# Kernel tuning notes

Measured on AMD Instinct MI355X. Metric: run time of the kernel, lower is better.

Reference implementation:

```python
import jax, jax.numpy as jnp
import numpy as np


def setup_inputs() -> dict:
    key = jax.random.key(0)
    k1, k2, k3 = jax.random.split(key, 3)
    b, n, h, d = 2, 2048, 16, 64
    q = jax.random.normal(k1, (b, n, h, d), dtype=jnp.float32)
    k = jax.random.normal(k2, (b, n, h, d), dtype=jnp.float32)
    v = jax.random.normal(k3, (b, n, h, d), dtype=jnp.float32)
    return {"q": q, "k": k, "v": v, "is_causal": 1}


def reference(q, k, v, is_causal):
    # q, k, v: [b, n, h, d]
    b, n, h, d = q.shape
    scale = 1.0 / jnp.sqrt(jnp.asarray(d, dtype=q.dtype))
    # scores: [b, h, n_q, n_k]
    scores = jnp.einsum("bqhd,bkhd->bhqk", q, k) * scale
    if is_causal:
        causal_mask = jnp.triu(jnp.ones((n, n), dtype=bool), k=1)  # True above diagonal
        scores = jnp.where(causal_mask[None, None, :, :], jnp.asarray(-jnp.inf, scores.dtype), scores)
    attn = jax.nn.softmax(scores, axis=-1)
    # output back to [b, n, h, d]
    out = jnp.einsum("bhqk,bkhd->bqhd", attn, v)
    return out
```

## Files before the change

### kernel.cpp

```cpp
#include <hip/hip_runtime.h>
#include <hip/hip_bf16.h>
#include <math.h>

typedef __bf16 bf16x8 __attribute__((ext_vector_type(8)));
typedef __bf16 bf16x4 __attribute__((ext_vector_type(4)));
typedef float  f32x4  __attribute__((ext_vector_type(4)));

#define KVBLK 64
#define HD    64
#define LDK   72
#define LDV   68
#define LDP   72
#define NQT   32

__global__ __launch_bounds__(256, 2)
void fattn_fwd(const float* __restrict__ Q, const float* __restrict__ K,
               const float* __restrict__ V, const int* __restrict__ causal_p,
               float* __restrict__ O, int B, int N, int H) {
  __shared__ alignas(16) __bf16 Kl[KVBLK][LDK];
  __shared__ alignas(16) __bf16 Vl[HD][LDV];
  __shared__ alignas(16) __bf16 Pl[64][LDP];

  const int tid  = threadIdx.x;
  const int wave = tid >> 6;
  const int lane = tid & 63;
  const int lo   = lane & 15;
  const int hi   = lane >> 4;

  const int xA = blockIdx.x;
  const int xB = NQT - 1 - xA;
  const int bh = blockIdx.y;
  const int bb = bh / H;
  const int hh = bh - bb * H;

  const int causal = causal_p[0];
  const int sN = H * HD;

  const float* Qb = Q + (long)bb * N * sN + hh * HD;
  const float* Kb = K + (long)bb * N * sN + hh * HD;
  const float* Vb = V + (long)bb * N * sN + hh * HD;
  float*       Ob = O + (long)bb * N * sN + hh * HD;

  const int tmaxA = causal ? xA : (NQT - 1);
  const int tmaxB = causal ? xB : (NQT - 1);

  const float qscale = 0.125f * 1.44269504088896340736f;
  bf16x8 aq[2][2];
#pragma unroll
  for (int qi = 0; qi < 2; ++qi) {
    const int q0q = ((qi == 0) ? xA : xB) * 64;
    const float* qp = Qb + (long)(q0q + wave * 16 + lo) * sN;
#pragma unroll
    for (int c = 0; c < 2; ++c) {
      f32x4 x0 = *(const f32x4*)(qp + c * 32 + hi * 8);
      f32x4 x1 = *(const f32x4*)(qp + c * 32 + hi * 8 + 4);
      bf16x8 a;
#pragma unroll
      for (int j = 0; j < 4; ++j) {
        a[j]     = (__bf16)(x0[j] * qscale);
        a[j + 4] = (__bf16)(x1[j] * qscale);
      }
      aq[qi][c] = a;
    }
  }

  f32x4 acc[2][4];
  float m_run[2][4], l_run[2][4];
#pragma unroll
  for (int qi = 0; qi < 2; ++qi)
#pragma unroll
    for (int i = 0; i < 4; ++i) {
      acc[qi][i] = (f32x4){0.f, 0.f, 0.f, 0.f};
      m_run[qi][i] = -INFINITY;
      l_run[qi][i] = 0.f;
    }

  f32x4 kreg[4], vreg[4];
  auto issue = [&](int tt) {
    const int k0 = tt * KVBLK;
#pragma unroll
    for (int i = 0; i < 4; ++i) {
      const int flat = tid + i * 256;
      const int r = flat >> 4, c4 = (flat & 15) * 4;
      kreg[i] = *(const f32x4*)(Kb + (long)(k0 + r) * sN + c4);
    }
    const float* vrow = Vb + (long)(k0 + wave * 16 + hi * 4) * sN + lo * 4;
#pragma unroll
    for (int q = 0; q < 4; ++q) vreg[q] = *(const f32x4*)(vrow + (long)q * sN);
  };
  auto wr = [&]() {
#pragma unroll
    for (int i = 0; i < 4; ++i) {
      const int flat = tid + i * 256;
      const int r = flat >> 4, c4 = (flat & 15) * 4;
      bf16x4 kb;
#pragma unroll
      for (int j = 0; j < 4; ++j) kb[j] = (__bf16)kreg[i][j];
      *(bf16x4*)&Kl[r][c4] = kb;
    }
#pragma unroll
    for (int j = 0; j < 4; ++j) {
      bf16x4 vv;
#pragma unroll
      for (int q = 0; q < 4; ++q) vv[q] = (__bf16)vreg[q][j];
      *(bf16x4*)&Vl[lo * 4 + j][wave * 16 + hi * 4] = vv;
    }
  };

  issue(0);
  wr();
  __syncthreads();

  for (int t = 0; t <= tmaxB; ++t) {
    const bool pf = (t < tmaxB);
    if (pf) issue(t + 1);
    const int k0 = t * KVBLK;

#pragma unroll
    for (int qi = 0; qi < 2; ++qi) {
      if (qi == 0 && t > tmaxA) continue;
      const int qt  = (qi == 0) ? xA : xB;
      const int q0q = qt * 64;

      f32x4 s[4];
#pragma unroll
      for (int nt = 0; nt < 4; ++nt) s[nt] = (f32x4){0.f, 0.f, 0.f, 0.f};
#pragma unroll
      for (int c = 0; c < 2; ++c) {
#pragma unroll
        for (int nt = 0; nt < 4; ++nt) {
          bf16x8 b = *(const bf16x8*)&Kl[nt * 16 + lo][c * 32 + hi * 8];
          s[nt] = __builtin_amdgcn_mfma_f32_16x16x32_bf16(aq[qi][c], b, s[nt], 0, 0, 0);
        }
      }

      if (causal && t == qt) {
#pragma unroll
        for (int nt = 0; nt < 4; ++nt) {
          const int kvg = k0 + nt * 16 + lo;
#pragma unroll
          for (int r = 0; r < 4; ++r) {
            const int qg = q0q + wave * 16 + hi * 4 + r;
            if (kvg > qg) s[nt][r] = -INFINITY;
          }
        }
      }

#pragma unroll
      for (int r = 0; r < 4; ++r) {
        float mx = fmaxf(fmaxf(s[0][r], s[1][r]), fmaxf(s[2][r], s[3][r]));
        mx = fmaxf(mx, __shfl_xor(mx, 1));
        mx = fmaxf(mx, __shfl_xor(mx, 2));
        mx = fmaxf(mx, __shfl_xor(mx, 4));
        mx = fmaxf(mx, __shfl_xor(mx, 8));
        const float mnew = fmaxf(m_run[qi][r], mx);
        const float fac  = exp2f(m_run[qi][r] - mnew);
        float ps = 0.f;
#pragma unroll
        for (int nt = 0; nt < 4; ++nt) {
          const float p = exp2f(s[nt][r] - mnew);
          s[nt][r] = p;
          ps += p;
        }
        ps += __shfl_xor(ps, 1);
        ps += __shfl_xor(ps, 2);
        ps += __shfl_xor(ps, 4);
        ps += __shfl_xor(ps, 8);
        l_run[qi][r] = l_run[qi][r] * fac + ps;
        m_run[qi][r] = mnew;
#pragma unroll
        for (int nt = 0; nt < 4; ++nt) acc[qi][nt][r] *= fac;
      }

      asm volatile("s_waitcnt lgkmcnt(0)" ::: "memory");
#pragma unroll
      for (int nt = 0; nt < 4; ++nt)
#pragma unroll
        for (int r = 0; r < 4; ++r)
          Pl[wave * 16 + hi * 4 + r][nt * 16 + lo] = (__bf16)s[nt][r];
      asm volatile("s_waitcnt lgkmcnt(0)" ::: "memory");

#pragma unroll
      for (int c = 0; c < 2; ++c) {
        bf16x8 pa = *(const bf16x8*)&Pl[wave * 16 + lo][c * 32 + hi * 8];
#pragma unroll
        for (int nt = 0; nt < 4; ++nt) {
          const __bf16* vp = &Vl[nt * 16 + lo][c * 32 + hi * 8];
          bf16x4 v0 = *(const bf16x4*)vp;
          bf16x4 v1 = *(const bf16x4*)(vp + 4);
          bf16x8 vb;
#pragma unroll
          for (int j = 0; j < 4; ++j) { vb[j] = v0[j]; vb[j + 4] = v1[j]; }
          acc[qi][nt] = __builtin_amdgcn_mfma_f32_16x16x32_bf16(pa, vb, acc[qi][nt], 0, 0, 0);
        }
      }
    }

    __syncthreads();
    if (pf) wr();
    __syncthreads();
  }

#pragma unroll
  for (int qi = 0; qi < 2; ++qi) {
    const int q0q = ((qi == 0) ? xA : xB) * 64;
    const int qrow = q0q + wave * 16 + hi * 4;
#pragma unroll
    for (int nt = 0; nt < 4; ++nt) {
#pragma unroll
      for (int r = 0; r < 4; ++r) {
        Ob[(long)(qrow + r) * sN + nt * 16 + lo] = acc[qi][nt][r] / l_run[qi][r];
      }
    }
  }
}

extern "C" void kernel_launch(void* const* d_in, const int* in_sizes, int n_in,
                              void* d_out, int out_size, void* d_ws, size_t ws_size,
                              hipStream_t stream) {
  const float* q = (const float*)d_in[0];
  const float* k = (const float*)d_in[1];
  const float* v = (const float*)d_in[2];
  const int* causal = (const int*)d_in[3];
  float* out = (float*)d_out;
  const int B = 2, N = 2048, H = 16;
  dim3 grid(NQT / 2, B * H);
  fattn_fwd<<<grid, dim3(256), 0, stream>>>(q, k, v, causal, out, B, N, H);
}
```

Baseline: 167.2 us.

## Split KV loop across two wave groups with split-softmax merge and swizzled LDS

```diff
diff --git a/kernel.cpp b/kernel.cpp
--- a/kernel.cpp
+++ b/kernel.cpp
@@ -6,32 +6,32 @@
 typedef __bf16 bf16x4 __attribute__((ext_vector_type(4)));
 typedef float  f32x4  __attribute__((ext_vector_type(4)));
 
-#define KVBLK 64
-#define HD    64
-#define LDK   72
-#define LDV   68
-#define LDP   72
-#define NQT   32
-
-__global__ __launch_bounds__(256, 2)
+#define HD  64
+#define NQT 32
+#define SWZ(r, c) ((c) ^ (((r) & 7) << 3))
+
+__global__ __launch_bounds__(512, 4)
 void fattn_fwd(const float* __restrict__ Q, const float* __restrict__ K,
                const float* __restrict__ V, const int* __restrict__ causal_p,
                float* __restrict__ O, int B, int N, int H) {
-  __shared__ alignas(16) __bf16 Kl[KVBLK][LDK];
-  __shared__ alignas(16) __bf16 Vl[HD][LDV];
-  __shared__ alignas(16) __bf16 Pl[64][LDP];
+  __shared__ union SMem {
+    struct { __bf16 K[2][64][64]; __bf16 V[2][64][64]; __bf16 P[2][64][64]; } t;
+    float mrg[24][2][256];
+  } sm;
 
   const int tid  = threadIdx.x;
-  const int wave = tid >> 6;
+  const int w    = tid >> 6;
+  const int g    = w >> 2;
+  const int w4   = w & 3;
   const int lane = tid & 63;
-  const int lo   = lane & 15;
-  const int hi   = lane >> 4;
-
-  const int xA = blockIdx.x;
+  const int lo = lane & 15, hi = lane >> 4;
+  const int t256 = tid & 255;
+
+  const int flat = (blockIdx.x & 7) * 64 + (blockIdx.x >> 3);
+  const int xA = flat & 15;
+  const int bh = flat >> 4;
   const int xB = NQT - 1 - xA;
-  const int bh = blockIdx.y;
-  const int bb = bh / H;
-  const int hh = bh - bb * H;
+  const int bb = bh / H, hh = bh - bb * H;
 
   const int causal = causal_p[0];
   const int sN = H * HD;
@@ -49,7 +49,7 @@
 #pragma unroll
   for (int qi = 0; qi < 2; ++qi) {
     const int q0q = ((qi == 0) ? xA : xB) * 64;
-    const float* qp = Qb + (long)(q0q + wave * 16 + lo) * sN;
+    const float* qp = Qb + (long)(q0q + w4 * 16 + lo) * sN;
 #pragma unroll
     for (int c = 0; c < 2; ++c) {
       f32x4 x0 = *(const f32x4*)(qp + c * 32 + hi * 8);
@@ -77,121 +77,127 @@
 
   f32x4 kreg[4], vreg[4];
   auto issue = [&](int tt) {
-    const int k0 = tt * KVBLK;
+    const int k0 = tt * 64;
 #pragma unroll
     for (int i = 0; i < 4; ++i) {
-      const int flat = tid + i * 256;
-      const int r = flat >> 4, c4 = (flat & 15) * 4;
+      const int fl = t256 + i * 256;
+      const int r = fl >> 4, c4 = (fl & 15) * 4;
       kreg[i] = *(const f32x4*)(Kb + (long)(k0 + r) * sN + c4);
     }
-    const float* vrow = Vb + (long)(k0 + wave * 16 + hi * 4) * sN + lo * 4;
+    const float* vrow = Vb + (long)(k0 + w4 * 16 + hi * 4) * sN + lo * 4;
 #pragma unroll
     for (int q = 0; q < 4; ++q) vreg[q] = *(const f32x4*)(vrow + (long)q * sN);
   };
   auto wr = [&]() {
 #pragma unroll
     for (int i = 0; i < 4; ++i) {
-      const int flat = tid + i * 256;
-      const int r = flat >> 4, c4 = (flat & 15) * 4;
+      const int fl = t256 + i * 256;
+      const int r = fl >> 4, c4 = (fl & 15) * 4;
       bf16x4 kb;
 #pragma unroll
       for (int j = 0; j < 4; ++j) kb[j] = (__bf16)kreg[i][j];
-      *(bf16x4*)&Kl[r][c4] = kb;
+      *(bf16x4*)&sm.t.K[g][r][SWZ(r, c4)] = kb;
     }
 #pragma unroll
     for (int j = 0; j < 4; ++j) {
+      const int d = lo * 4 + j;
       bf16x4 vv;
 #pragma unroll
       for (int q = 0; q < 4; ++q) vv[q] = (__bf16)vreg[q][j];
-      *(bf16x4*)&Vl[lo * 4 + j][wave * 16 + hi * 4] = vv;
+      *(bf16x4*)&sm.t.V[g][d][SWZ(d, w4 * 16 + hi * 4)] = vv;
     }
   };
 
-  issue(0);
+  issue(g);
   wr();
   __syncthreads();
 
-  for (int t = 0; t <= tmaxB; ++t) {
-    const bool pf = (t < tmaxB);
-    if (pf) issue(t + 1);
-    const int k0 = t * KVBLK;
-
-#pragma unroll
-    for (int qi = 0; qi < 2; ++qi) {
-      if (qi == 0 && t > tmaxA) continue;
-      const int qt  = (qi == 0) ? xA : xB;
-      const int q0q = qt * 64;
-
-      f32x4 s[4];
-#pragma unroll
-      for (int nt = 0; nt < 4; ++nt) s[nt] = (f32x4){0.f, 0.f, 0.f, 0.f};
-#pragma unroll
-      for (int c = 0; c < 2; ++c) {
-#pragma unroll
-        for (int nt = 0; nt < 4; ++nt) {
-          bf16x8 b = *(const bf16x8*)&Kl[nt * 16 + lo][c * 32 + hi * 8];
-          s[nt] = __builtin_amdgcn_mfma_f32_16x16x32_bf16(aq[qi][c], b, s[nt], 0, 0, 0);
-        }
-      }
-
-      if (causal && t == qt) {
-#pragma unroll
-        for (int nt = 0; nt < 4; ++nt) {
-          const int kvg = k0 + nt * 16 + lo;
+  const int niter = (tmaxB >> 1) + 1;
+  for (int i = 0; i < niter; ++i) {
+    const int tg = 2 * i + g;
+    const bool active = (tg <= tmaxB);
+    const bool pf = (tg + 2 <= tmaxB);
+    if (pf) issue(tg + 2);
+
+    if (active) {
+      const int k0 = tg * 64;
+#pragma unroll
+      for (int qi = 0; qi < 2; ++qi) {
+        const int qt = (qi == 0) ? xA : xB;
+        if (qi == 0 && tg > tmaxA) continue;
+        const int q0q = qt * 64;
+
+        f32x4 s[4];
+#pragma unroll
+        for (int nt = 0; nt < 4; ++nt) s[nt] = (f32x4){0.f, 0.f, 0.f, 0.f};
+#pragma unroll
+        for (int c = 0; c < 2; ++c) {
+#pragma unroll
+          for (int nt = 0; nt < 4; ++nt) {
+            const int kr = nt * 16 + lo;
+            bf16x8 b = *(const bf16x8*)&sm.t.K[g][kr][SWZ(kr, c * 32 + hi * 8)];
+            s[nt] = __builtin_amdgcn_mfma_f32_16x16x32_bf16(aq[qi][c], b, s[nt], 0, 0, 0);
+          }
+        }
+
+        if (causal && tg == qt) {
+#pragma unroll
+          for (int nt = 0; nt < 4; ++nt) {
+            const int kvg = k0 + nt * 16 + lo;
+#pragma unroll
+            for (int r = 0; r < 4; ++r) {
+              const int qg = q0q + w4 * 16 + hi * 4 + r;
+              if (kvg > qg) s[nt][r] = -INFINITY;
+            }
+          }
+        }
+
+#pragma unroll
+        for (int r = 0; r < 4; ++r) {
+          float mx = fmaxf(fmaxf(s[0][r], s[1][r]), fmaxf(s[2][r], s[3][r]));
+          mx = fmaxf(mx, __shfl_xor(mx, 1));
+          mx = fmaxf(mx, __shfl_xor(mx, 2));
+          mx = fmaxf(mx, __shfl_xor(mx, 4));
+          mx = fmaxf(mx, __shfl_xor(mx, 8));
+          const float mnew = fmaxf(m_run[qi][r], mx);
+          const float fac  = exp2f(m_run[qi][r] - mnew);
+          float ps = 0.f;
+#pragma unroll
+          for (int nt = 0; nt < 4; ++nt) {
+            const float p = exp2f(s[nt][r] - mnew);
+            s[nt][r] = p;
+            ps += p;
+          }
+          ps += __shfl_xor(ps, 1);
+          ps += __shfl_xor(ps, 2);
+          ps += __shfl_xor(ps, 4);
+          ps += __shfl_xor(ps, 8);
+          l_run[qi][r] = l_run[qi][r] * fac + ps;
+          m_run[qi][r] = mnew;
+#pragma unroll
+          for (int nt = 0; nt < 4; ++nt) acc[qi][nt][r] *= fac;
+        }
+
+        asm volatile("s_waitcnt lgkmcnt(0)" ::: "memory");
+#pragma unroll
+        for (int nt = 0; nt < 4; ++nt)
 #pragma unroll
           for (int r = 0; r < 4; ++r) {
-            const int qg = q0q + wave * 16 + hi * 4 + r;
-            if (kvg > qg) s[nt][r] = -INFINITY;
-          }
-        }
-      }
-
-#pragma unroll
-      for (int r = 0; r < 4; ++r) {
-        float mx = fmaxf(fmaxf(s[0][r], s[1][r]), fmaxf(s[2][r], s[3][r]));
-        mx = fmaxf(mx, __shfl_xor(mx, 1));
-        mx = fmaxf(mx, __shfl_xor(mx, 2));
-        mx = fmaxf(mx, __shfl_xor(mx, 4));
-        mx = fmaxf(mx, __shfl_xor(mx, 8));
-        const float mnew = fmaxf(m_run[qi][r], mx);
-        const float fac  = exp2f(m_run[qi][r] - mnew);
-        float ps = 0.f;
-#pragma unroll
-        for (int nt = 0; nt < 4; ++nt) {
-          const float p = exp2f(s[nt][r] - mnew);
-          s[nt][r] = p;
-          ps += p;
-        }
-        ps += __shfl_xor(ps, 1);
-        ps += __shfl_xor(ps, 2);
-        ps += __shfl_xor(ps, 4);
-        ps += __shfl_xor(ps, 8);
-        l_run[qi][r] = l_run[qi][r] * fac + ps;
-        m_run[qi][r] = mnew;
-#pragma unroll
-        for (int nt = 0; nt < 4; ++nt) acc[qi][nt][r] *= fac;
-      }
-
-      asm volatile("s_waitcnt lgkmcnt(0)" ::: "memory");
-#pragma unroll
-      for (int nt = 0; nt < 4; ++nt)
-#pragma unroll
-        for (int r = 0; r < 4; ++r)
-          Pl[wave * 16 + hi * 4 + r][nt * 16 + lo] = (__bf16)s[nt][r];
-      asm volatile("s_waitcnt lgkmcnt(0)" ::: "memory");
-
-#pragma unroll
-      for (int c = 0; c < 2; ++c) {
-        bf16x8 pa = *(const bf16x8*)&Pl[wave * 16 + lo][c * 32 + hi * 8];
-#pragma unroll
-        for (int nt = 0; nt < 4; ++nt) {
-          const __bf16* vp = &Vl[nt * 16 + lo][c * 32 + hi * 8];
-          bf16x4 v0 = *(const bf16x4*)vp;
-          bf16x4 v1 = *(const bf16x4*)(vp + 4);
-          bf16x8 vb;
-#pragma unroll
-          for (int j = 0; j < 4; ++j) { vb[j] = v0[j]; vb[j + 4] = v1[j]; }
-          acc[qi][nt] = __builtin_amdgcn_mfma_f32_16x16x32_bf16(pa, vb, acc[qi][nt], 0, 0, 0);
+            const int q = w4 * 16 + hi * 4 + r;
+            sm.t.P[g][q][SWZ(q, nt * 16 + lo)] = (__bf16)s[nt][r];
+          }
+        asm volatile("s_waitcnt lgkmcnt(0)" ::: "memory");
+
+#pragma unroll
+        for (int c = 0; c < 2; ++c) {
+          const int pr = w4 * 16 + lo;
+          bf16x8 pa = *(const bf16x8*)&sm.t.P[g][pr][SWZ(pr, c * 32 + hi * 8)];
+#pragma unroll
+          for (int nt = 0; nt < 4; ++nt) {
+            const int vr2 = nt * 16 + lo;
+            bf16x8 vb = *(const bf16x8*)&sm.t.V[g][vr2][SWZ(vr2, c * 32 + hi * 8)];
+            acc[qi][nt] = __builtin_amdgcn_mfma_f32_16x16x32_bf16(pa, vb, acc[qi][nt], 0, 0, 0);
+          }
         }
       }
     }
@@ -201,16 +207,49 @@
     __syncthreads();
   }
 
-#pragma unroll
-  for (int qi = 0; qi < 2; ++qi) {
-    const int q0q = ((qi == 0) ? xA : xB) * 64;
-    const int qrow = q0q + wave * 16 + hi * 4;
-#pragma unroll
-    for (int nt = 0; nt < 4; ++nt) {
+  __syncthreads();
+  const int cidx = w4 * 64 + lane;
+  if (g == 1) {
+#pragma unroll
+    for (int qi = 0; qi < 2; ++qi) {
+#pragma unroll
+      for (int nt = 0; nt < 4; ++nt)
+#pragma unroll
+        for (int r = 0; r < 4; ++r)
+          sm.mrg[nt * 4 + r][qi][cidx] = acc[qi][nt][r];
 #pragma unroll
       for (int r = 0; r < 4; ++r) {
-        Ob[(long)(qrow + r) * sN + nt * 16 + lo] = acc[qi][nt][r] / l_run[qi][r];
-      }
+        sm.mrg[16 + r][qi][cidx] = m_run[qi][r];
+        sm.mrg[20 + r][qi][cidx] = l_run[qi][r];
+      }
+    }
+  }
+  __syncthreads();
+  if (g == 0) {
+#pragma unroll
+    for (int qi = 0; qi < 2; ++qi) {
+      const int q0q = ((qi == 0) ? xA : xB) * 64;
+      float f1[4], f2[4], linv[4];
+#pragma unroll
+      for (int r = 0; r < 4; ++r) {
+        const float m2 = sm.mrg[16 + r][qi][cidx];
+        const float l2 = sm.mrg[20 + r][qi][cidx];
+        const float m1 = m_run[qi][r], l1 = l_run[qi][r];
+        const float mm = fmaxf(m1, m2);
+        const float e1 = (m1 == -INFINITY) ? 0.f : exp2f(m1 - mm);
+        const float e2 = (m2 == -INFINITY) ? 0.f : exp2f(m2 - mm);
+        f1[r] = e1; f2[r] = e2;
+        linv[r] = 1.f / (l1 * e1 + l2 * e2);
+      }
+      const int qrow = q0q + w4 * 16 + hi * 4;
+#pragma unroll
+      for (int nt = 0; nt < 4; ++nt)
+#pragma unroll
+        for (int r = 0; r < 4; ++r) {
+          const float a2 = sm.mrg[nt * 4 + r][qi][cidx];
+          Ob[(long)(qrow + r) * sN + nt * 16 + lo] =
+            (acc[qi][nt][r] * f1[r] + a2 * f2[r]) * linv[r];
+        }
     }
   }
 }
@@ -224,6 +263,6 @@
   const int* causal = (const int*)d_in[3];
   float* out = (float*)d_out;
   const int B = 2, N = 2048, H = 16;
-  dim3 grid(NQT / 2, B * H);
-  fattn_fwd<<<grid, dim3(256), 0, stream>>>(q, k, v, causal, out, B, N, H);
+  dim3 grid((NQT / 2) * B * H);
+  fattn_fwd<<<grid, dim3(512), 0, stream>>>(q, k, v, causal, out, B, N, H);
 }
```

Result: slower. 367.7 us (+120.0%).
